# Performance work log

Measured on AMD Instinct MI355X. Metric: run time of the kernel, lower is better.

## Reference

```python
import jax, jax.numpy as jnp
import numpy as np

EPS = 1e-5

def _ln(x, g, b):
    m = jnp.mean(x, axis=-1, keepdims=True)
    v = jnp.var(x, axis=-1, keepdims=True)
    return (x - m) / jnp.sqrt(v + EPS) * g + b

def _partition(x, nw):
    b, h, w, c = x.shape
    x = x.reshape(b, nw, h // nw, nw, w // nw, c).transpose(0, 1, 3, 2, 4, 5)
    return x.reshape(b * nw * nw, h // nw, w // nw, c)

def _merge(x, nw):
    b_, h, w, c = x.shape
    b = b_ // (nw * nw)
    x = x.reshape(b, nw, nw, h, w, c).transpose(0, 1, 3, 2, 4, 5)
    return x.reshape(b, nw * h, nw * w, c)

def _window_attn(q, k, v, width, height, nw, mask):
    b, _, c = q.shape
    q = q.reshape(b, height, width, c)
    k = k.reshape(b, height, width, c)
    v = v.reshape(b, height, width, c)
    sh, sw = (height // nw) // 2, (width // nw) // 2
    q = jnp.roll(q, (-sh, -sw), (1, 2))
    k = jnp.roll(k, (-sh, -sw), (1, 2))
    v = jnp.roll(v, (-sh, -sw), (1, 2))
    q = _partition(q, nw); k = _partition(k, nw); v = _partition(v, nw)
    N = (height // nw) * (width // nw)
    b_ = b * nw * nw
    qf = q.reshape(b_, N, c); kf = k.reshape(b_, N, c); vf = v.reshape(b_, N, c)
    scale = jnp.asarray(c, qf.dtype) ** 0.5
    scores = jnp.einsum('bnc,bmc->bnm', qf, kf) / scale  # [b_, N, N]
    scores = (scores.reshape(b, nw * nw, N, N) + mask[None]).reshape(b_, N, N)
    attn = jax.nn.softmax(scores, axis=-1)
    out = jnp.einsum('bnm,bmc->bnc', attn, vf)
    out = _merge(out.reshape(b_, height // nw, width // nw, c), nw)
    out = jnp.roll(out, (sh, sw), (1, 2))
    return out.reshape(b, height * width, c)

def _block(feat0, feat1, width, height, mask, nw, wq, wk, wv, wfc, g, be, ffn=None):
    q = feat0 @ wq; k = feat1 @ wk; v = feat1 @ wv
    a = _window_attn(q, k, v, width, height, nw, mask)
    a = _ln(a @ wfc, g, be)
    if ffn is not None:
        w1, w2, fg, fb = ffn
        h = jax.nn.gelu(jnp.concatenate([feat0, a], axis=-1) @ w1, approximate=False)
        a = _ln(h @ w2, fg, fb)
    return feat0 + a

def setup_inputs() -> dict:
    key = jax.random.key(0)
    B, H, W, NW, D = 8, 128, 128, 8, 256
    N = (H // NW) * (W // NW)
    ks = jax.random.split(key, 16)
    s = D ** -0.5
    return {
        'feat0': jax.random.normal(ks[0], (B, H * W, D), jnp.float32),
        'feat1': jax.random.normal(ks[1], (B, H * W, D), jnp.float32),
        'mask_attn': jax.random.normal(ks[2], (NW * NW, N, N), jnp.float32),
        'width': W, 'height': H, 'n_window': NW,
        'intra_wq': jax.random.normal(ks[3], (D, D), jnp.float32) * s,
        'intra_wk': jax.random.normal(ks[4], (D, D), jnp.float32) * s,
        'intra_wv': jax.random.normal(ks[5], (D, D), jnp.float32) * s,
        'intra_wfc': jax.random.normal(ks[6], (D, D), jnp.float32) * s,
        'intra_g': jnp.ones((D,), jnp.float32),
        'intra_b': jnp.zeros((D,), jnp.float32),
        'inter_wq': jax.random.normal(ks[7], (D, D), jnp.float32) * s,
        'inter_wk': jax.random.normal(ks[8], (D, D), jnp.float32) * s,
        'inter_wv': jax.random.normal(ks[9], (D, D), jnp.float32) * s,
        'inter_wfc': jax.random.normal(ks[10], (D, D), jnp.float32) * s,
        'inter_g': jnp.ones((D,), jnp.float32),
        'inter_b': jnp.zeros((D,), jnp.float32),
        'inter_w1': jax.random.normal(ks[11], (2 * D, 2 * D * 4), jnp.float32) * (2 * D) ** -0.5,
        'inter_w2': jax.random.normal(ks[12], (2 * D * 4, D), jnp.float32) * (2 * D * 4) ** -0.5,
        'inter_fg': jnp.ones((D,), jnp.float32),
        'inter_fb': jnp.zeros((D,), jnp.float32),
    }

def reference(feat0, feat1, mask_attn, width, height, n_window,
              intra_wq, intra_wk, intra_wv, intra_wfc, intra_g, intra_b,
              inter_wq, inter_wk, inter_wv, inter_wfc, inter_g, inter_b,
              inter_w1, inter_w2, inter_fg, inter_fb):
    f0 = _block(feat0, feat0, width, height, mask_attn, n_window,
                intra_wq, intra_wk, intra_wv, intra_wfc, intra_g, intra_b)
    out = _block(f0, feat1, width, height, mask_attn, n_window,
                 inter_wq, inter_wk, inter_wv, inter_wfc, inter_g, inter_b,
                 ffn=(inter_w1, inter_w2, inter_fg, inter_fb))
    return out
```

## Files before the change

kernel.cpp:

```cpp
#include <hip/hip_runtime.h>

typedef unsigned short u16;
typedef unsigned int   u32;

using f32x4  = __attribute__((ext_vector_type(4))) float;
using bf16x8 = __attribute__((ext_vector_type(8))) __bf16;

__device__ inline u16 f2bf(float f) {
  return __builtin_bit_cast(u16, (__bf16)f);
}
__device__ inline float bf2f(u16 v) {
  u32 u = ((u32)v) << 16;
  return __builtin_bit_cast(float, u);
}

__device__ inline void gl_lds16(const u16* g, u16* l) {
  __builtin_amdgcn_global_load_lds((const __attribute__((address_space(1))) void*)g,
                                   (__attribute__((address_space(3))) void*)l,
                                   16, 0, 0);
}

__device__ inline int perm_fwd(int m) {
  int b = m >> 14, rem = m & 16383;
  int h = rem >> 7, w = rem & 127;
  int hr = (h - 8) & 127, wr = (w - 8) & 127;
  int win = (b << 6) | ((hr >> 4) << 3) | (wr >> 4);
  return (win << 8) | ((hr & 15) << 4) | (wr & 15);
}
__device__ inline int perm_inv(int r) {
  int win = r >> 8, t = r & 255;
  int b = win >> 6, wy = (win >> 3) & 7, wx = win & 7;
  int h = (((wy << 4) | (t >> 4)) + 8) & 127;
  int w = (((wx << 4) | (t & 15)) + 8) & 127;
  return (b << 14) | (h << 7) | w;
}


enum { MODE_QKV = 0, MODE_PV = 2, MODE_FFN1 = 4 };

template<int MODE>
__global__ __launch_bounds__(256)
void gemm_nt(const u16* __restrict__ A, int lda, long long sAz,
             const u16* __restrict__ Bt, int ldb, long long sBz,
             u16* __restrict__ OutB, float* __restrict__ OutF,
             const float* __restrict__ mask, int K, int ldo)
{
  __shared__ __align__(16) u16 sA[128 * 64];
  __shared__ __align__(16) u16 sB[128 * 64];

  const int tid  = threadIdx.x;
  const int lane = tid & 63;
  const int wave = tid >> 6;
  const int l15  = lane & 15;
  const int quad = lane >> 4;
  const int wm   = (wave >> 1) << 6;
  const int wn   = (wave & 1) << 6;
  const int z    = blockIdx.z;
  const int m0   = (int)(blockIdx.y) << 7;
  const int n0   = (int)(blockIdx.x) << 7;

  const u16* Ab = A  + (long long)z * sAz;
  const u16* Bb = Bt + (long long)z * sBz;

  const int cd = ((lane & 7) ^ ((lane >> 3) & 7)) << 3;
  const int rs = (wave << 5) + (lane >> 3);
  const u16* ga0 = Ab + (long long)(m0 + rs) * lda + cd;
  const u16* gb0 = Bb + (long long)(n0 + rs) * ldb + cd;
  u16* la0 = &sA[wave << 11];
  u16* lb0 = &sB[wave << 11];

  const f32x4 zero = {0.f, 0.f, 0.f, 0.f};
  f32x4 acc[4][4];
#pragma unroll
  for (int i = 0; i < 4; ++i)
#pragma unroll
    for (int j = 0; j < 4; ++j) acc[i][j] = zero;

  for (int k0 = 0; k0 < K; k0 += 64) {
    __syncthreads();
#pragma unroll
    for (int p = 0; p < 4; ++p) {
      gl_lds16(ga0 + k0 + (p << 3) * lda, la0 + (p << 9));
      gl_lds16(gb0 + k0 + (p << 3) * ldb, lb0 + (p << 9));
    }
    __syncthreads();
#pragma unroll
    for (int kk = 0; kk < 2; ++kk) {
      const int sw = (((quad | (kk << 2)) ^ (l15 & 7)) << 3);
      bf16x8 af[4], bfr[4];
#pragma unroll
      for (int i = 0; i < 4; ++i) {
        af[i]  = *(const bf16x8*)(sA + ((wm + (i << 4) + l15) << 6) + sw);
        bfr[i] = *(const bf16x8*)(sB + ((wn + (i << 4) + l15) << 6) + sw);
      }
#pragma unroll
      for (int i = 0; i < 4; ++i)
#pragma unroll
        for (int j = 0; j < 4; ++j)
          acc[i][j] = __builtin_amdgcn_mfma_f32_16x16x32_bf16(af[i], bfr[j], acc[i][j], 0, 0, 0);
    }
  }

#pragma unroll
  for (int i = 0; i < 4; ++i) {
#pragma unroll
    for (int r = 0; r < 4; ++r) {
      int mg = m0 + wm + (i << 4) + (quad << 2) + r;
      if constexpr (MODE == MODE_QKV) {
        u16* orow = OutB + (long long)(n0 >> 8) * ldo + ((long long)perm_fwd(mg) << 8);
#pragma unroll
        for (int j = 0; j < 4; ++j) {
          int ng = n0 + wn + (j << 4) + l15;
          orow[ng & 255] = f2bf(acc[i][j][r]);
        }
      } else if constexpr (MODE == MODE_PV) {
        u16* orow = OutB + ((long long)perm_inv((z << 8) + mg) << 8);
#pragma unroll
        for (int j = 0; j < 4; ++j) {
          int ng = n0 + wn + (j << 4) + l15;
          orow[ng] = f2bf(acc[i][j][r]);
        }
      } else {
        u16* orow = OutB + (long long)mg * ldo;
#pragma unroll
        for (int j = 0; j < 4; ++j) {
          int ng = n0 + wn + (j << 4) + l15;
          float v = acc[i][j][r];
          float t = v * fmaf(v * v, -0.071354816f, -1.5957691216f);
          float g = v * __builtin_amdgcn_rcpf(1.0f + __expf(t));
          orow[ng] = f2bf(g);
        }
      }
    }
  }
}

__global__ __launch_bounds__(256)
void gemm_vt(const u16* __restrict__ Wt,
             const u16* __restrict__ Feat,
             u16* __restrict__ Vt)
{
  __shared__ __align__(16) u16 sA[128 * 64];
  __shared__ __align__(16) u16 sB[128 * 64];

  const int tid  = threadIdx.x;
  const int lane = tid & 63;
  const int wave = tid >> 6;
  const int l15  = lane & 15;
  const int quad = lane >> 4;
  const int wm   = (wave >> 1) << 6;
  const int wn   = (wave & 1) << 6;
  const int z    = blockIdx.z;
  const int m0   = (int)(blockIdx.y) << 7;
  const int n0   = (int)(blockIdx.x) << 7;

  const int cd = ((lane & 7) ^ ((lane >> 3) & 7)) << 3;
  const int rs = (wave << 5) + (lane >> 3);
  const u16* ga0 = Wt + (long long)(m0 + rs) * 256 + cd;
  const u16* gb0 = Feat + (long long)perm_inv((z << 8) + n0 + rs)        * 256 + cd;
  const u16* gb1 = Feat + (long long)perm_inv((z << 8) + n0 + rs + 8)    * 256 + cd;
  const u16* gb2 = Feat + (long long)perm_inv((z << 8) + n0 + rs + 16)   * 256 + cd;
  const u16* gb3 = Feat + (long long)perm_inv((z << 8) + n0 + rs + 24)   * 256 + cd;
  u16* la0 = &sA[wave << 11];
  u16* lb0 = &sB[wave << 11];

  const f32x4 zero = {0.f, 0.f, 0.f, 0.f};
  f32x4 acc[4][4];
#pragma unroll
  for (int i = 0; i < 4; ++i)
#pragma unroll
    for (int j = 0; j < 4; ++j) acc[i][j] = zero;

  for (int k0 = 0; k0 < 256; k0 += 64) {
    __syncthreads();
#pragma unroll
    for (int p = 0; p < 4; ++p)
      gl_lds16(ga0 + k0 + (p << 3) * 256, la0 + (p << 9));
    gl_lds16(gb0 + k0, lb0);
    gl_lds16(gb1 + k0, lb0 + 512);
    gl_lds16(gb2 + k0, lb0 + 1024);
    gl_lds16(gb3 + k0, lb0 + 1536);
    __syncthreads();
#pragma unroll
    for (int kk = 0; kk < 2; ++kk) {
      const int sw = (((quad | (kk << 2)) ^ (l15 & 7)) << 3);
      bf16x8 af[4], bfr[4];
#pragma unroll
      for (int i = 0; i < 4; ++i) {
        af[i]  = *(const bf16x8*)(sA + ((wm + (i << 4) + l15) << 6) + sw);
        bfr[i] = *(const bf16x8*)(sB + ((wn + (i << 4) + l15) << 6) + sw);
      }
#pragma unroll
      for (int i = 0; i < 4; ++i)
#pragma unroll
        for (int j = 0; j < 4; ++j)
          acc[i][j] = __builtin_amdgcn_mfma_f32_16x16x32_bf16(af[i], bfr[j], acc[i][j], 0, 0, 0);
    }
  }

#pragma unroll
  for (int i = 0; i < 4; ++i) {
#pragma unroll
    for (int r = 0; r < 4; ++r) {
      const int mg = m0 + wm + (i << 4) + (quad << 2) + r;
      u16* orow = Vt + (((long long)z) << 16) + ((long long)mg << 8);
#pragma unroll
      for (int j = 0; j < 4; ++j) {
        int ng = n0 + wn + (j << 4) + l15;
        orow[ng] = f2bf(acc[i][j][r]);
      }
    }
  }
}

__global__ __launch_bounds__(256)
void scores_softmax(const u16* __restrict__ Q, const u16* __restrict__ Kw,
                    const float* __restrict__ mask, u16* __restrict__ SP)
{
  __shared__ __align__(16) u16 sA[128 * 64];
  __shared__ __align__(16) u16 sB[256 * 64];

  const int tid  = threadIdx.x;
  const int lane = tid & 63;
  const int wave = tid >> 6;
  const int l15  = lane & 15;
  const int quad = lane >> 4;

  const int mhalf = (int)blockIdx.x;
  const int z     = (int)blockIdx.y;
  const int m0    = mhalf << 7;

  const u16* Ab = Q  + ((long long)z << 16);
  const u16* Bb = Kw + ((long long)z << 16);

  const int cd  = ((lane & 7) ^ ((lane >> 3) & 7)) << 3;
  const int rsA = (wave << 5) + (lane >> 3);
  const int rsB = (wave << 6) + (lane >> 3);
  const u16* ga0 = Ab + (long long)(m0 + rsA) * 256 + cd;
  const u16* gb0 = Bb + (long long)rsB * 256 + cd;
  u16* la0 = &sA[wave << 11];
  u16* lb0 = &sB[wave << 12];

  const f32x4 zero = {0.f, 0.f, 0.f, 0.f};
  f32x4 acc[2][16];
#pragma unroll
  for (int i = 0; i < 2; ++i)
#pragma unroll
    for (int j = 0; j < 16; ++j) acc[i][j] = zero;

  for (int k0 = 0; k0 < 256; k0 += 64) {
    __syncthreads();
#pragma unroll
    for (int p = 0; p < 4; ++p)
      gl_lds16(ga0 + k0 + (p << 3) * 256, la0 + (p << 9));
#pragma unroll
    for (int p = 0; p < 8; ++p)
      gl_lds16(gb0 + k0 + (p << 3) * 256, lb0 + (p << 9));
    __syncthreads();
#pragma unroll
    for (int kk = 0; kk < 2; ++kk) {
      const int sw = (((quad | (kk << 2)) ^ (l15 & 7)) << 3);
      bf16x8 af0 = *(const bf16x8*)(sA + (((wave << 5) + l15) << 6) + sw);
      bf16x8 af1 = *(const bf16x8*)(sA + (((wave << 5) + 16 + l15) << 6) + sw);
#pragma unroll
      for (int j = 0; j < 16; ++j) {
        bf16x8 bf = *(const bf16x8*)(sB + (((j << 4) + l15) << 6) + sw);
        acc[0][j] = __builtin_amdgcn_mfma_f32_16x16x32_bf16(af0, bf, acc[0][j], 0, 0, 0);
        acc[1][j] = __builtin_amdgcn_mfma_f32_16x16x32_bf16(af1, bf, acc[1][j], 0, 0, 0);
      }
    }
  }

  const float* mbase = mask + (((long long)(z & 63)) << 16);
#pragma unroll
  for (int i = 0; i < 2; ++i) {
#pragma unroll
    for (int r = 0; r < 4; ++r) {
      const int mg = m0 + (wave << 5) + (i << 4) + (quad << 2) + r;
      const float* mrow = mbase + ((long long)mg << 8);
      float sv[16];
      float mx = -3.0e38f;
#pragma unroll
      for (int j = 0; j < 16; ++j) {
        sv[j] = acc[i][j][r] * 0.0625f + mrow[(j << 4) + l15];
        mx = fmaxf(mx, sv[j]);
      }
#pragma unroll
      for (int o = 1; o < 16; o <<= 1) mx = fmaxf(mx, __shfl_xor(mx, o));
      float sum = 0.f;
#pragma unroll
      for (int j = 0; j < 16; ++j) { sv[j] = __expf(sv[j] - mx); sum += sv[j]; }
#pragma unroll
      for (int o = 1; o < 16; o <<= 1) sum += __shfl_xor(sum, o);
      const float inv = 1.0f / sum;
      u16* orow = SP + (((long long)z) << 16) + ((long long)mg << 8);
#pragma unroll
      for (int j = 0; j < 16; ++j) orow[(j << 4) + l15] = f2bf(sv[j] * inv);
    }
  }
}

enum { LN_XCAT0 = 0, LN_XCAT1 = 1, LN_OUT = 2 };

template<int MODE>
__global__ __launch_bounds__(256)
void gemm_ln(const u16* __restrict__ A, int lda,
             const u16* __restrict__ Bt,
             const float* __restrict__ G, const float* __restrict__ Bias,
             const float* __restrict__ ResF, const u16* __restrict__ ResB,
             float* __restrict__ OutF, u16* __restrict__ OutB, int K)
{
  __shared__ __align__(16) u16 sA[64 * 64];
  __shared__ __align__(16) u16 sB[256 * 64];

  const int tid  = threadIdx.x;
  const int lane = tid & 63;
  const int wave = tid >> 6;
  const int l15  = lane & 15;
  const int quad = lane >> 4;
  const int m0   = (int)blockIdx.x << 6;

  const int cd  = ((lane & 7) ^ ((lane >> 3) & 7)) << 3;
  const int rsA = (wave << 4) + (lane >> 3);
  const int rsB = (wave << 6) + (lane >> 3);
  const u16* ga0 = A  + (long long)(m0 + rsA) * lda + cd;
  const u16* gb0 = Bt + (long long)rsB * K + cd;
  u16* la0 = &sA[wave << 10];
  u16* lb0 = &sB[wave << 12];

  const f32x4 zero = {0.f, 0.f, 0.f, 0.f};
  f32x4 acc[16];
#pragma unroll
  for (int j = 0; j < 16; ++j) acc[j] = zero;

  for (int k0 = 0; k0 < K; k0 += 64) {
    __syncthreads();
#pragma unroll
    for (int p = 0; p < 2; ++p)
      gl_lds16(ga0 + k0 + (p << 3) * lda, la0 + (p << 9));
#pragma unroll
    for (int p = 0; p < 8; ++p)
      gl_lds16(gb0 + k0 + (p << 3) * K, lb0 + (p << 9));
    __syncthreads();
#pragma unroll
    for (int kk = 0; kk < 2; ++kk) {
      const int sw = (((quad | (kk << 2)) ^ (l15 & 7)) << 3);
      bf16x8 af = *(const bf16x8*)(sA + (((wave << 4) + l15) << 6) + sw);
#pragma unroll
      for (int j = 0; j < 16; ++j) {
        bf16x8 bf = *(const bf16x8*)(sB + (((j << 4) + l15) << 6) + sw);
        acc[j] = __builtin_amdgcn_mfma_f32_16x16x32_bf16(af, bf, acc[j], 0, 0, 0);
      }
    }
  }

  float gj[16], bj[16];
#pragma unroll
  for (int j = 0; j < 16; ++j) {
    gj[j] = G[(j << 4) + l15];
    bj[j] = Bias[(j << 4) + l15];
  }

#pragma unroll
  for (int r = 0; r < 4; ++r) {
    const int mg = m0 + (wave << 4) + (quad << 2) + r;
    float s = 0.f, s2 = 0.f;
#pragma unroll
    for (int j = 0; j < 16; ++j) {
      float v = acc[j][r];
      s += v; s2 += v * v;
    }
#pragma unroll
    for (int o = 1; o < 16; o <<= 1) { s += __shfl_xor(s, o); s2 += __shfl_xor(s2, o); }
    const float mean = s * (1.0f / 256.0f);
    const float var  = s2 * (1.0f / 256.0f) - mean * mean;
    const float rstd = rsqrtf(var + 1e-5f);
    if constexpr (MODE == LN_XCAT0) {
      u16* orow = OutB + ((long long)mg << 9);
      const float* rrow = ResF + ((long long)mg << 8);
#pragma unroll
      for (int j = 0; j < 16; ++j) {
        float v = (acc[j][r] - mean) * rstd * gj[j] + bj[j];
        orow[(j << 4) + l15] = f2bf(v + rrow[(j << 4) + l15]);
      }
    } else if constexpr (MODE == LN_XCAT1) {
      u16* orow = OutB + ((long long)mg << 9) + 256;
#pragma unroll
      for (int j = 0; j < 16; ++j) {
        float v = (acc[j][r] - mean) * rstd * gj[j] + bj[j];
        orow[(j << 4) + l15] = f2bf(v);
      }
    } else {
      const u16* rrow = ResB + ((long long)mg << 9);
      float* orow = OutF + ((long long)mg << 8);
#pragma unroll
      for (int j = 0; j < 16; ++j) {
        float v = (acc[j][r] - mean) * rstd * gj[j] + bj[j];
        orow[(j << 4) + l15] = v + bf2f(rrow[(j << 4) + l15]);
      }
    }
  }
}

__global__ __launch_bounds__(256)
void cvt_f32_bf16(const float* __restrict__ src, u16* __restrict__ dst, int n4)
{
  int i = blockIdx.x * 256 + threadIdx.x;
  if (i >= n4) return;
  float4 v = ((const float4*)src)[i];
  ushort4 u; u.x = f2bf(v.x); u.y = f2bf(v.y); u.z = f2bf(v.z); u.w = f2bf(v.w);
  ((ushort4*)dst)[i] = u;
}

__global__ __launch_bounds__(256)
void wtrans(const float* __restrict__ src, u16* __restrict__ dst, int R, int C)
{
  int idx = blockIdx.x * 256 + threadIdx.x;
  if (idx >= R * C) return;
  int r = idx / C, c = idx - r * C;
  dst[c * R + r] = f2bf(src[idx]);
}

extern "C" void kernel_launch(void* const* d_in, const int* in_sizes, int n_in,
                              void* d_out, int out_size, void* d_ws, size_t ws_size,
                              hipStream_t stream)
{
  (void)in_sizes; (void)n_in; (void)out_size;
  const float* feat0 = (const float*)d_in[0];
  const float* feat1 = (const float*)d_in[1];
  const float* mask  = (const float*)d_in[2];
  const float* wq1 = (const float*)d_in[6];
  const float* wk1 = (const float*)d_in[7];
  const float* wv1 = (const float*)d_in[8];
  const float* wf1 = (const float*)d_in[9];
  const float* g1  = (const float*)d_in[10];
  const float* b1  = (const float*)d_in[11];
  const float* wq2 = (const float*)d_in[12];
  const float* wk2 = (const float*)d_in[13];
  const float* wv2 = (const float*)d_in[14];
  const float* wf2 = (const float*)d_in[15];
  const float* g2  = (const float*)d_in[16];
  const float* b2  = (const float*)d_in[17];
  const float* w1  = (const float*)d_in[18];
  const float* w2  = (const float*)d_in[19];
  const float* fg  = (const float*)d_in[20];
  const float* fb  = (const float*)d_in[21];

  const size_t Mi = 1048576;
  const size_t WB = 4 * Mi;
  const int Mtot = 131072;

  int nc = 8;
  for (int c = 1; c <= 8; c <<= 1) {
    size_t S = (size_t)(Mtot / c) * 512;
    if (7 * S + WB <= ws_size) { nc = c; break; }
  }
  const int Mc = Mtot / nc;
  const size_t S = (size_t)Mc * 512;

  char* ws = (char*)d_ws;
  u16*   featb = (u16*)(ws);
  u16*   SPb   = featb;
  u16*   qw    = (u16*)(ws + S);
  u16*   Ob    = qw;
  u16*   hbuf  = featb;
  u16*   kw    = (u16*)(ws + 2 * S);
  u16*   vt    = (u16*)(ws + 4 * S);
  u16*   xcat  = (u16*)(ws + 5 * S);
  u16*   wb    = (u16*)(ws + 7 * S);
  u16* wq1t = wb;            u16* wk1t = wb + 65536;  u16* wv1t = wb + 131072; u16* wf1t = wb + 196608;
  u16* wq2t = wb + 262144;   u16* wk2t = wb + 327680; u16* wv2t = wb + 393216; u16* wf2t = wb + 458752;
  u16* w1t  = wb + 524288;
  u16* w2t  = wb + 524288 + 1048576;

  const dim3 blk(256);
  const dim3 gBig(2, Mc / 128, 1);
  const dim3 gQK(4, Mc / 128, 1);
  const int  Wc = Mc / 256;
  const dim3 gWin(2, 2, Wc);
  const dim3 gSS(2, Wc);
  const int  gRows = Mc / 4;
  const int  gLN   = Mc / 64;
  const int  MF = Mc / 2;
  const dim3 gF1(16, MF / 128, 1);
  const int  gLNF  = MF / 64;

  wtrans<<<256, blk, 0, stream>>>(wq1, wq1t, 256, 256);
  wtrans<<<256, blk, 0, stream>>>(wk1, wk1t, 256, 256);
  wtrans<<<256, blk, 0, stream>>>(wv1, wv1t, 256, 256);
  wtrans<<<256, blk, 0, stream>>>(wf1, wf1t, 256, 256);
  wtrans<<<256, blk, 0, stream>>>(wq2, wq2t, 256, 256);
  wtrans<<<256, blk, 0, stream>>>(wk2, wk2t, 256, 256);
  wtrans<<<256, blk, 0, stream>>>(wv2, wv2t, 256, 256);
  wtrans<<<256, blk, 0, stream>>>(wf2, wf2t, 256, 256);
  wtrans<<<4096, blk, 0, stream>>>(w1, w1t, 512, 2048);
  wtrans<<<2048, blk, 0, stream>>>(w2, w2t, 2048, 256);

  const int qkStride = Mc * 256;

  for (int c = 0; c < nc; ++c) {
    const long long off = (long long)c * Mc * 256;
    const float* f0in = feat0 + off;
    const float* f1in = feat1 + off;
    float* outp = (float*)d_out + off;

    cvt_f32_bf16<<<gRows, blk, 0, stream>>>(f0in, featb, Mc * 64);
    gemm_nt<MODE_QKV><<<gQK, blk, 0, stream>>>(featb, 256, 0, wq1t, 256, 0, qw, nullptr, nullptr, 256, qkStride);
    gemm_vt<<<gWin, blk, 0, stream>>>(wv1t, featb, vt);
    scores_softmax<<<gSS, blk, 0, stream>>>(qw, kw, mask, SPb);
    gemm_nt<MODE_PV><<<gWin, blk, 0, stream>>>(SPb, 256, 65536, vt, 256, 65536, Ob, nullptr, nullptr, 256, 0);
    gemm_ln<LN_XCAT0><<<gLN, blk, 0, stream>>>(Ob, 256, wf1t, g1, b1, f0in, nullptr, nullptr, xcat, 256);

    cvt_f32_bf16<<<gRows, blk, 0, stream>>>(f1in, featb, Mc * 64);
    gemm_nt<MODE_QKV><<<gBig, blk, 0, stream>>>(xcat, 512, 0, wq2t, 256, 0, qw, nullptr, nullptr, 512, 0);
    gemm_nt<MODE_QKV><<<gBig, blk, 0, stream>>>(featb, 256, 0, wk2t, 256, 0, kw, nullptr, nullptr, 256, 0);
    gemm_vt<<<gWin, blk, 0, stream>>>(wv2t, featb, vt);
    scores_softmax<<<gSS, blk, 0, stream>>>(qw, kw, mask, SPb);
    gemm_nt<MODE_PV><<<gWin, blk, 0, stream>>>(SPb, 256, 65536, vt, 256, 65536, Ob, nullptr, nullptr, 256, 0);
    gemm_ln<LN_XCAT1><<<gLN, blk, 0, stream>>>(Ob, 256, wf2t, g2, b2, nullptr, nullptr, nullptr, xcat, 256);

    for (int mc = 0; mc < 2; ++mc) {
      const u16* xc = xcat + (long long)mc * MF * 512;
      gemm_nt<MODE_FFN1><<<gF1, blk, 0, stream>>>(xc, 512, 0, w1t, 512, 0,
                                                  hbuf, nullptr, nullptr, 512, 2048);
      gemm_ln<LN_OUT><<<gLNF, blk, 0, stream>>>(hbuf, 2048, w2t, fg, fb, nullptr,
                                                xcat + (long long)mc * MF * 512,
                                                outp + (long long)mc * MF * 256, nullptr, 2048);
    }
  }
}
```

Before: 1.633 ms.

## Double gemm_ln row tile and vectorize GELU stores via permuted W2 layout

The GEMM+LayerNorm kernel now processes 128 rows per block instead of 64. Each wave computes two 16-row MFMA tiles that share the same B-operand LDS reads, which halves the B-matrix reloads per output row. The GELU epilogue of the FFN-up GEMM now packs four outputs into one 8-byte store using v_cvt_pk_bf16_f32. To keep the FFN-down contraction consistent with that packed layout, W2 is transposed with a matching permutation of its K index. The cost is more accumulator registers and half as many blocks in the LN GEMMs.

After: 1.757 ms. +7.6%, slower.

```diff
diff --git a/kernel.cpp b/kernel.cpp
--- a/kernel.cpp
+++ b/kernel.cpp
@@ -12,6 +12,11 @@
 __device__ inline float bf2f(u16 v) {
   u32 u = ((u32)v) << 16;
   return __builtin_bit_cast(float, u);
+}
+__device__ inline u32 pk_bf16(float a, float b) {
+  u32 d;
+  asm("v_cvt_pk_bf16_f32 %0, %1, %2" : "=v"(d) : "v"(a), "v"(b));
+  return d;
 }
 
 __device__ inline void gl_lds16(const u16* g, u16* l) {
@@ -121,15 +126,17 @@
           orow[ng] = f2bf(acc[i][j][r]);
         }
       } else {
-        u16* orow = OutB + (long long)mg * ldo;
+        float gv[4];
 #pragma unroll
         for (int j = 0; j < 4; ++j) {
-          int ng = n0 + wn + (j << 4) + l15;
           float v = acc[i][j][r];
           float t = v * fmaf(v * v, -0.071354816f, -1.5957691216f);
-          float g = v * __builtin_amdgcn_rcpf(1.0f + __expf(t));
-          orow[ng] = f2bf(g);
+          gv[j] = v * __builtin_amdgcn_rcpf(1.0f + __expf(t));
         }
+        uint2 d;
+        d.x = pk_bf16(gv[0], gv[1]);
+        d.y = pk_bf16(gv[2], gv[3]);
+        *(uint2*)(OutB + (long long)mg * ldo + n0 + wn + (l15 << 2)) = d;
       }
     }
   }
@@ -310,7 +317,7 @@
              const float* __restrict__ ResF, const u16* __restrict__ ResB,
              float* __restrict__ OutF, u16* __restrict__ OutB, int K)
 {
-  __shared__ __align__(16) u16 sA[64 * 64];
+  __shared__ __align__(16) u16 sA[128 * 64];
   __shared__ __align__(16) u16 sB[256 * 64];
 
   const int tid  = threadIdx.x;
@@ -318,25 +325,27 @@
   const int wave = tid >> 6;
   const int l15  = lane & 15;
   const int quad = lane >> 4;
-  const int m0   = (int)blockIdx.x << 6;
+  const int m0   = (int)blockIdx.x << 7;
 
   const int cd  = ((lane & 7) ^ ((lane >> 3) & 7)) << 3;
-  const int rsA = (wave << 4) + (lane >> 3);
+  const int rsA = (wave << 5) + (lane >> 3);
   const int rsB = (wave << 6) + (lane >> 3);
   const u16* ga0 = A  + (long long)(m0 + rsA) * lda + cd;
   const u16* gb0 = Bt + (long long)rsB * K + cd;
-  u16* la0 = &sA[wave << 10];
+  u16* la0 = &sA[wave << 11];
   u16* lb0 = &sB[wave << 12];
 
   const f32x4 zero = {0.f, 0.f, 0.f, 0.f};
-  f32x4 acc[16];
-#pragma unroll
-  for (int j = 0; j < 16; ++j) acc[j] = zero;
+  f32x4 acc[2][16];
+#pragma unroll
+  for (int i = 0; i < 2; ++i)
+#pragma unroll
+    for (int j = 0; j < 16; ++j) acc[i][j] = zero;
 
   for (int k0 = 0; k0 < K; k0 += 64) {
     __syncthreads();
 #pragma unroll
-    for (int p = 0; p < 2; ++p)
+    for (int p = 0; p < 4; ++p)
       gl_lds16(ga0 + k0 + (p << 3) * lda, la0 + (p << 9));
 #pragma unroll
     for (int p = 0; p < 8; ++p)
@@ -345,11 +354,13 @@
 #pragma unroll
     for (int kk = 0; kk < 2; ++kk) {
       const int sw = (((quad | (kk << 2)) ^ (l15 & 7)) << 3);
-      bf16x8 af = *(const bf16x8*)(sA + (((wave << 4) + l15) << 6) + sw);
+      bf16x8 af0 = *(const bf16x8*)(sA + (((wave << 5) + l15) << 6) + sw);
+      bf16x8 af1 = *(const bf16x8*)(sA + (((wave << 5) + 16 + l15) << 6) + sw);
 #pragma unroll
       for (int j = 0; j < 16; ++j) {
         bf16x8 bf = *(const bf16x8*)(sB + (((j << 4) + l15) << 6) + sw);
-        acc[j] = __builtin_amdgcn_mfma_f32_16x16x32_bf16(af, bf, acc[j], 0, 0, 0);
+        acc[0][j] = __builtin_amdgcn_mfma_f32_16x16x32_bf16(af0, bf, acc[0][j], 0, 0, 0);
+        acc[1][j] = __builtin_amdgcn_mfma_f32_16x16x32_bf16(af1, bf, acc[1][j], 0, 0, 0);
       }
     }
   }
@@ -362,41 +373,44 @@
   }
 
 #pragma unroll
-  for (int r = 0; r < 4; ++r) {
-    const int mg = m0 + (wave << 4) + (quad << 2) + r;
-    float s = 0.f, s2 = 0.f;
-#pragma unroll
-    for (int j = 0; j < 16; ++j) {
-      float v = acc[j][r];
-      s += v; s2 += v * v;
-    }
-#pragma unroll
-    for (int o = 1; o < 16; o <<= 1) { s += __shfl_xor(s, o); s2 += __shfl_xor(s2, o); }
-    const float mean = s * (1.0f / 256.0f);
-    const float var  = s2 * (1.0f / 256.0f) - mean * mean;
-    const float rstd = rsqrtf(var + 1e-5f);
-    if constexpr (MODE == LN_XCAT0) {
-      u16* orow = OutB + ((long long)mg << 9);
-      const float* rrow = ResF + ((long long)mg << 8);
+  for (int i = 0; i < 2; ++i) {
+#pragma unroll
+    for (int r = 0; r < 4; ++r) {
+      const int mg = m0 + (wave << 5) + (i << 4) + (quad << 2) + r;
+      float s = 0.f, s2 = 0.f;
 #pragma unroll
       for (int j = 0; j < 16; ++j) {
-        float v = (acc[j][r] - mean) * rstd * gj[j] + bj[j];
-        orow[(j << 4) + l15] = f2bf(v + rrow[(j << 4) + l15]);
-      }
-    } else if constexpr (MODE == LN_XCAT1) {
-      u16* orow = OutB + ((long long)mg << 9) + 256;
-#pragma unroll
-      for (int j = 0; j < 16; ++j) {
-        float v = (acc[j][r] - mean) * rstd * gj[j] + bj[j];
-        orow[(j << 4) + l15] = f2bf(v);
-      }
-    } else {
-      const u16* rrow = ResB + ((long long)mg << 9);
-      float* orow = OutF + ((long long)mg << 8);
-#pragma unroll
-      for (int j = 0; j < 16; ++j) {
-        float v = (acc[j][r] - mean) * rstd * gj[j] + bj[j];
-        orow[(j << 4) + l15] = v + bf2f(rrow[(j << 4) + l15]);
+        float v = acc[i][j][r];
+        s += v; s2 += v * v;
+      }
+#pragma unroll
+      for (int o = 1; o < 16; o <<= 1) { s += __shfl_xor(s, o); s2 += __shfl_xor(s2, o); }
+      const float mean = s * (1.0f / 256.0f);
+      const float var  = s2 * (1.0f / 256.0f) - mean * mean;
+      const float rstd = rsqrtf(var + 1e-5f);
+      if constexpr (MODE == LN_XCAT0) {
+        u16* orow = OutB + ((long long)mg << 9);
+        const float* rrow = ResF + ((long long)mg << 8);
+#pragma unroll
+        for (int j = 0; j < 16; ++j) {
+          float v = (acc[i][j][r] - mean) * rstd * gj[j] + bj[j];
+          orow[(j << 4) + l15] = f2bf(v + rrow[(j << 4) + l15]);
+        }
+      } else if constexpr (MODE == LN_XCAT1) {
+        u16* orow = OutB + ((long long)mg << 9) + 256;
+#pragma unroll
+        for (int j = 0; j < 16; ++j) {
+          float v = (acc[i][j][r] - mean) * rstd * gj[j] + bj[j];
+          orow[(j << 4) + l15] = f2bf(v);
+        }
+      } else {
+        const u16* rrow = ResB + ((long long)mg << 9);
+        float* orow = OutF + ((long long)mg << 8);
+#pragma unroll
+        for (int j = 0; j < 16; ++j) {
+          float v = (acc[i][j][r] - mean) * rstd * gj[j] + bj[j];
+          orow[(j << 4) + l15] = v + bf2f(rrow[(j << 4) + l15]);
+        }
       }
     }
   }
@@ -419,6 +433,15 @@
   if (idx >= R * C) return;
   int r = idx / C, c = idx - r * C;
   dst[c * R + r] = f2bf(src[idx]);
+}
+
+__global__ __launch_bounds__(256)
+void wtrans_w2(const float* __restrict__ src, u16* __restrict__ dst)
+{
+  int idx = blockIdx.x * 256 + threadIdx.x;
+  int c = idx >> 11, q = idx & 2047;
+  int f = (q & ~63) | ((q & 3) << 4) | ((q >> 2) & 15);
+  dst[idx] = f2bf(src[f * 256 + c]);
 }
 
 extern "C" void kernel_launch(void* const* d_in, const int* in_sizes, int n_in,
@@ -480,10 +503,10 @@
   const dim3 gWin(2, 2, Wc);
   const dim3 gSS(2, Wc);
   const int  gRows = Mc / 4;
-  const int  gLN   = Mc / 64;
+  const int  gLN   = Mc / 128;
   const int  MF = Mc / 2;
   const dim3 gF1(16, MF / 128, 1);
-  const int  gLNF  = MF / 64;
+  const int  gLNF  = MF / 128;
 
   wtrans<<<256, blk, 0, stream>>>(wq1, wq1t, 256, 256);
   wtrans<<<256, blk, 0, stream>>>(wk1, wk1t, 256, 256);
@@ -494,7 +517,7 @@
   wtrans<<<256, blk, 0, stream>>>(wv2, wv2t, 256, 256);
   wtrans<<<256, blk, 0, stream>>>(wf2, wf2t, 256, 256);
   wtrans<<<4096, blk, 0, stream>>>(w1, w1t, 512, 2048);
-  wtrans<<<2048, blk, 0, stream>>>(w2, w2t, 2048, 256);
+  wtrans_w2<<<2048, blk, 0, stream>>>(w2, w2t);
 
   const int qkStride = Mc * 256;
 
```
